# Kernel optimization log

Hardware: AMD Instinct MI355X
Metric: run time of the kernel (lower is better)

Reference implementation:

```python
import jax, jax.numpy as jnp
import numpy as np

T = 4096      # tokens
H = 1024      # hidden_size
I = 4096      # intermediate_size
E = 8         # num_experts


def setup_inputs() -> dict:
    key = jax.random.key(0)
    ks = jax.random.split(key, 6)
    s_h = 1.0 / np.sqrt(H)
    s_i = 1.0 / np.sqrt(I)
    return {
        "x":  jax.random.normal(ks[0], (T, H), dtype=jnp.float32),
        "Wg": jax.random.uniform(ks[1], (E, H), jnp.float32, -s_h, s_h),   # gate: Linear(H, E), no bias
        "W1": jax.random.uniform(ks[2], (E, H, I), jnp.float32, -s_h, s_h),
        "b1": jax.random.uniform(ks[3], (E, I), jnp.float32, -s_h, s_h),
        "W2": jax.random.uniform(ks[4], (E, I, H), jnp.float32, -s_i, s_i),
        "b2": jax.random.uniform(ks[5], (E, H), jnp.float32, -s_i, s_i),
    }


def reference(x, Wg, W1, b1, W2, b2):
    # Gate: softmax over experts. gate_scores: [T, E]
    gate_scores = jax.nn.softmax(x @ Wg.T, axis=-1)
    # All experts run densely on all tokens (batched GEMMs).
    h = jax.nn.gelu(jnp.einsum('th,ehi->eti', x, W1) + b1[:, None, :],
                    approximate=False)                      # [E, T, I]
    y = jnp.einsum('eti,eih->eth', h, W2) + b2[:, None, :]  # [E, T, H]
    # Gate-weighted sum over experts (fuses the stack + mul + sum).
    return jnp.einsum('te,eth->th', gate_scores, y)         # [T, H]
```

## Files before the change

### kernel.cpp

```cpp
#include <hip/hip_runtime.h>
#include <math.h>

#define T_TOK 4096
#define H_DIM 1024
#define I_DIM 4096
#define E_NUM 8
#define KEI   32768


typedef short s16x8 __attribute__((ext_vector_type(8)));
typedef float f32x4 __attribute__((ext_vector_type(4)));

__device__ __forceinline__ unsigned short f2b(float f) {
  union { float f; unsigned u; } v; v.f = f;
  unsigned r = v.u + 0x7fffu + ((v.u >> 16) & 1u);
  return (unsigned short)(r >> 16);
}

__device__ __forceinline__ void gld_lds16(short* lds, const short* g) {
  __builtin_amdgcn_global_load_lds(
      (const __attribute__((address_space(1))) void*)g,
      (__attribute__((address_space(3))) void*)lds, 16, 0, 0);
}

__device__ __forceinline__ float gelu_f(float v) {
  float a = fabsf(v);
  float z = a * 0.70710678118f;
  float t = __builtin_amdgcn_rcpf(fmaf(0.47047f, z, 1.0f));
  float p = fmaf(fmaf(0.7478556f, t, -0.0958798f), t, 0.3480242f) * t;
  float e = __expf(-z * z);
  float erf_abs = fmaf(-p, e, 1.0f);
  return fmaf(0.5f * a, erf_abs, 0.5f * v);
}

__global__ __launch_bounds__(256) void gate_kernel(
    const float* __restrict__ x, const float* __restrict__ Wg,
    float* __restrict__ gate)
{
  int t = blockIdx.x * 4 + (threadIdx.x >> 6);
  int lane = threadIdx.x & 63;
  const float* xr = x + (size_t)t * H_DIM;
  float acc[E_NUM];
#pragma unroll
  for (int e = 0; e < E_NUM; ++e) acc[e] = 0.f;
  for (int j = 0; j < H_DIM / 64; ++j) {
    float xv = xr[lane + j * 64];
#pragma unroll
    for (int e = 0; e < E_NUM; ++e)
      acc[e] += xv * Wg[e * H_DIM + lane + j * 64];
  }
#pragma unroll
  for (int e = 0; e < E_NUM; ++e)
    for (int s = 32; s > 0; s >>= 1)
      acc[e] += __shfl_xor(acc[e], s, 64);
  if (lane == 0) {
    float mx = acc[0];
#pragma unroll
    for (int e = 1; e < E_NUM; ++e) mx = fmaxf(mx, acc[e]);
    float sum = 0.f, ex[E_NUM];
#pragma unroll
    for (int e = 0; e < E_NUM; ++e) { ex[e] = expf(acc[e] - mx); sum += ex[e]; }
    float inv = 1.f / sum;
#pragma unroll
    for (int e = 0; e < E_NUM; ++e) gate[t * E_NUM + e] = ex[e] * inv;
  }
}

__global__ __launch_bounds__(256) void convert_x_kernel(
    const float* __restrict__ x, short* __restrict__ xb)
{
  int rb = blockIdx.x;
  int t  = threadIdx.x & 63;
  int kq = threadIdx.x >> 6;
#pragma unroll
  for (int j = 0; j < 8; ++j) {
    int kc = blockIdx.y * 32 + kq + j * 4;
    const float* src = x + ((size_t)rb * 64 + t) * H_DIM + kc * 8;
    float4 a = *(const float4*)src;
    float4 b = *(const float4*)(src + 4);
    s16x8 v;
    v[0] = f2b(a.x); v[1] = f2b(a.y); v[2] = f2b(a.z); v[3] = f2b(a.w);
    v[4] = f2b(b.x); v[5] = f2b(b.y); v[6] = f2b(b.z); v[7] = f2b(b.w);
    *(s16x8*)(xb + ((size_t)rb * 128 + kc) * 512 + t * 8) = v;
  }
}

__global__ __launch_bounds__(256) void trans_w1_kernel(
    const float* __restrict__ W1, short* __restrict__ W1t)
{
  __shared__ short tile[64][65];
  int e = blockIdx.z;
  int i0 = blockIdx.x * 64, h0 = blockIdx.y * 64;
  int tid = threadIdx.x, c = tid & 63, r0 = tid >> 6;
  const float* src = W1 + ((size_t)e * H_DIM + h0) * I_DIM + i0;
#pragma unroll
  for (int j = 0; j < 16; ++j) {
    int r = j * 4 + r0;
    tile[r][c] = f2b(src[(size_t)r * I_DIM + c]);
  }
  __syncthreads();
  int i = tid & 63, kq = tid >> 6;
#pragma unroll
  for (int w = 0; w < 2; ++w) {
    int kcl = kq + w * 4;
    s16x8 v;
#pragma unroll
    for (int j = 0; j < 8; ++j) v[j] = tile[kcl * 8 + j][i];
    size_t chunk = (size_t)e * 8192 + (size_t)blockIdx.x * 128 + (h0 >> 3) + kcl;
    *(s16x8*)(W1t + chunk * 512 + i * 8) = v;
  }
}

__global__ __launch_bounds__(256) void trans_w2_kernel(
    const float* __restrict__ W2, short* __restrict__ W2t)
{
  __shared__ short tile[64][65];
  int e = blockIdx.z;
  int i0 = blockIdx.x * 64, h0 = blockIdx.y * 64;
  int tid = threadIdx.x, c = tid & 63, r0 = tid >> 6;
  const float* src = W2 + ((size_t)e * I_DIM + i0) * H_DIM + h0;
#pragma unroll
  for (int j = 0; j < 16; ++j) {
    int r = j * 4 + r0;
    tile[r][c] = f2b(src[(size_t)r * H_DIM + c]);
  }
  __syncthreads();
  int h = tid & 63, kq = tid >> 6;
#pragma unroll
  for (int w = 0; w < 2; ++w) {
    int kcl = kq + w * 4;
    s16x8 v;
#pragma unroll
    for (int j = 0; j < 8; ++j) v[j] = tile[kcl * 8 + j][h];
    size_t chunk = (size_t)blockIdx.y * 4096 + e * 512 + (i0 >> 3) + kcl;
    *(s16x8*)(W2t + chunk * 512 + h * 8) = v;
  }
}

__global__ __launch_bounds__(256) void out_init_kernel(
    const float* __restrict__ gate, const float* __restrict__ b2,
    float* __restrict__ out)
{
  int idx = blockIdx.x * 256 + threadIdx.x;
  int t = idx >> 10, h = idx & 1023;
  float v = 0.f;
#pragma unroll
  for (int e = 0; e < E_NUM; ++e)
    v += gate[t * E_NUM + e] * b2[e * H_DIM + h];
  out[idx] = v;
}

__global__ __launch_bounds__(256, 4) void gemm1_kernel(
    const short* __restrict__ xb, const short* __restrict__ W1t,
    const float* __restrict__ b1, const float* __restrict__ gate,
    short* __restrict__ hg)
{
  __shared__ __align__(16) short As[2 * 4096];
  __shared__ __align__(16) short Bs[2 * 4096];
  int bm = blockIdx.x, bn = blockIdx.y, e = blockIdx.z;

  const int tid = threadIdx.x, wave = tid >> 6, lane = tid & 63;
  const int wm = wave >> 1, wn = wave & 1;
  const int g = lane >> 4, r16 = lane & 15;

  f32x4 acc[4][4];
#pragma unroll
  for (int i = 0; i < 4; ++i)
#pragma unroll
    for (int j = 0; j < 4; ++j) acc[i][j] = (f32x4){0.f, 0.f, 0.f, 0.f};

  const int rbl = wave & 1, kq = wave >> 1;
  short* AsD0 = As + (kq * 128 + rbl * 64) * 8;
  short* AsD1 = As + ((kq + 2) * 128 + rbl * 64) * 8;
  short* BsD0 = Bs + (kq * 128 + rbl * 64) * 8;
  short* BsD1 = Bs + ((kq + 2) * 128 + rbl * 64) * 8;
  const short* Asrc = xb + (((size_t)(bm * 2 + rbl) * 128) + kq) * 512 + lane * 8;
  const short* Bsrc = W1t + (size_t)e * (8192 * 512)
                    + (((size_t)(bn * 2 + rbl) * 128) + kq) * 512 + lane * 8;

  gld_lds16(AsD0, Asrc);
  gld_lds16(AsD1, Asrc + 1024);
  gld_lds16(BsD0, Bsrc);
  gld_lds16(BsD1, Bsrc + 1024);

  for (int k0 = 0; k0 < H_DIM; k0 += 32) {
    int cur = (k0 >> 5) & 1;
    __syncthreads();
    if (k0 + 32 < H_DIM) {
      int nb = cur ^ 1;
      size_t soff = ((size_t)(k0 >> 3) + 4) * 512;
      gld_lds16(AsD0 + nb * 4096, Asrc + soff);
      gld_lds16(AsD1 + nb * 4096, Asrc + soff + 1024);
      gld_lds16(BsD0 + nb * 4096, Bsrc + soff);
      gld_lds16(BsD1 + nb * 4096, Bsrc + soff + 1024);
    }
    const short* Ab = As + cur * 4096;
    const short* Bb = Bs + cur * 4096;
    s16x8 af[4], bfr[4];
#pragma unroll
    for (int mi = 0; mi < 4; ++mi)
      af[mi] = *(const s16x8*)(Bb + ((g << 7) + (wm << 6) + (mi << 4) + r16) * 8);
#pragma unroll
    for (int ni = 0; ni < 4; ++ni)
      bfr[ni] = *(const s16x8*)(Ab + ((g << 7) + (wn << 6) + (ni << 4) + r16) * 8);
#pragma unroll
    for (int mi = 0; mi < 4; ++mi)
#pragma unroll
      for (int ni = 0; ni < 4; ++ni)
        acc[mi][ni] = __builtin_amdgcn_mfma_f32_16x16x32_bf16(
            af[mi], bfr[ni], acc[mi][ni], 0, 0, 0);
  }

  int n_base0 = bn * 128 + wm * 64;
  int t_base  = bm * 128 + wn * 64;
  float gt[4];
#pragma unroll
  for (int ni = 0; ni < 4; ++ni)
    gt[ni] = gate[(t_base + ni * 16 + r16) * E_NUM + e];
#pragma unroll
  for (int mi = 0; mi < 4; ++mi) {
    int nb = n_base0 + mi * 16 + g * 4;
    float4 b1v = *(const float4*)(b1 + e * I_DIM + nb);
    int k = e * I_DIM + nb;
    size_t koff = (size_t)(k >> 3) * 512 + (k & 7);
#pragma unroll
    for (int ni = 0; ni < 4; ++ni) {
      int t = t_base + ni * 16 + r16;
      float v0 = gelu_f(acc[mi][ni][0] + b1v.x) * gt[ni];
      float v1 = gelu_f(acc[mi][ni][1] + b1v.y) * gt[ni];
      float v2 = gelu_f(acc[mi][ni][2] + b1v.z) * gt[ni];
      float v3 = gelu_f(acc[mi][ni][3] + b1v.w) * gt[ni];
      int2 pk;
      pk.x = (int)((unsigned)f2b(v0) | ((unsigned)f2b(v1) << 16));
      pk.y = (int)((unsigned)f2b(v2) | ((unsigned)f2b(v3) << 16));
      *(int2*)(hg + (size_t)(t >> 6) * (4096 * 512) + koff + (size_t)(t & 63) * 8) = pk;
    }
  }
}

__global__ __launch_bounds__(256) void gemm2_kernel(
    const short* __restrict__ hg, const short* __restrict__ W2t,
    float* __restrict__ out)
{
  __shared__ __align__(16) short As[2 * 4096];
  __shared__ __align__(16) short Bs[2 * 8192];

  int bn = blockIdx.x;
  int bm = blockIdx.y;
  int ks = blockIdx.z;

  const int tid = threadIdx.x, wave = tid >> 6, lane = tid & 63;
  const int wm = wave >> 1, wn = wave & 1;
  const int g = lane >> 4, r16 = lane & 15;

  f32x4 acc[4][8];
#pragma unroll
  for (int i = 0; i < 4; ++i)
#pragma unroll
    for (int j = 0; j < 8; ++j) acc[i][j] = (f32x4){0.f, 0.f, 0.f, 0.f};

  const int kq = wave;
  short* AsD[2];
  const short* Asrc[2];
#pragma unroll
  for (int r = 0; r < 2; ++r) {
    AsD[r]  = As + (kq * 128 + r * 64) * 8;
    Asrc[r] = hg + (((size_t)(bm * 2 + r) * 4096) + kq) * 512 + lane * 8;
  }
  short* BsD[4];
  const short* Bsrc[4];
#pragma unroll
  for (int r = 0; r < 4; ++r) {
    BsD[r]  = Bs + (kq * 256 + r * 64) * 8;
    Bsrc[r] = W2t + (((size_t)(bn * 4 + r) * 4096) + kq) * 512 + lane * 8;
  }

  const int kBeg = ks * (KEI / 8), kEnd = kBeg + (KEI / 8);

  {
    size_t soff = (size_t)(kBeg >> 3) * 512;
#pragma unroll
    for (int r = 0; r < 2; ++r) gld_lds16(AsD[r], Asrc[r] + soff);
#pragma unroll
    for (int r = 0; r < 4; ++r) gld_lds16(BsD[r], Bsrc[r] + soff);
  }

  for (int k0 = kBeg; k0 < kEnd; k0 += 32) {
    int cur = ((k0 - kBeg) >> 5) & 1;
    __syncthreads();
    if (k0 + 32 < kEnd) {
      int nb = cur ^ 1;
      size_t soff = ((size_t)(k0 >> 3) + 4) * 512;
#pragma unroll
      for (int r = 0; r < 2; ++r) gld_lds16(AsD[r] + nb * 4096, Asrc[r] + soff);
#pragma unroll
      for (int r = 0; r < 4; ++r) gld_lds16(BsD[r] + nb * 8192, Bsrc[r] + soff);
    }
    const short* Ab = As + cur * 4096;
    const short* Bb = Bs + cur * 8192;
    s16x8 af[4], bfr[8];
#pragma unroll
    for (int mi = 0; mi < 4; ++mi)
      af[mi] = *(const s16x8*)(Ab + ((g << 7) + (wm << 6) + (mi << 4) + r16) * 8);
#pragma unroll
    for (int ni = 0; ni < 8; ++ni)
      bfr[ni] = *(const s16x8*)(Bb + ((g << 8) + (wn << 7) + (ni << 4) + r16) * 8);
#pragma unroll
    for (int mi = 0; mi < 4; ++mi)
#pragma unroll
      for (int ni = 0; ni < 8; ++ni)
        acc[mi][ni] = __builtin_amdgcn_mfma_f32_16x16x32_bf16(
            af[mi], bfr[ni], acc[mi][ni], 0, 0, 0);
  }

  int row0 = bm * 128 + wm * 64;
  int col0 = bn * 256 + wn * 128;
#pragma unroll
  for (int mi = 0; mi < 4; ++mi) {
#pragma unroll
    for (int r = 0; r < 4; ++r) {
      int t = row0 + mi * 16 + g * 4 + r;
#pragma unroll
      for (int ni = 0; ni < 8; ++ni) {
        int h = col0 + ni * 16 + r16;
        atomicAdd(&out[(size_t)t * H_DIM + h], acc[mi][ni][r]);
      }
    }
  }
}

extern "C" void kernel_launch(void* const* d_in, const int* in_sizes, int n_in,
                              void* d_out, int out_size, void* d_ws, size_t ws_size,
                              hipStream_t stream) {
  const float* x  = (const float*)d_in[0];
  const float* Wg = (const float*)d_in[1];
  const float* W1 = (const float*)d_in[2];
  const float* b1 = (const float*)d_in[3];
  const float* W2 = (const float*)d_in[4];
  const float* b2 = (const float*)d_in[5];
  float* out = (float*)d_out;

  char* ws = (char*)d_ws;
  float* gate = (float*)ws;
  short* xb   = (short*)(ws + 131072);
  short* W1t  = (short*)(ws + 131072 + 8388608);
  short* W2t  = (short*)(ws + 131072 + 8388608 + 67108864);
  short* hg   = (short*)(ws + 131072 + 8388608 + 2 * 67108864);

  gate_kernel<<<T_TOK / 4, 256, 0, stream>>>(x, Wg, gate);
  convert_x_kernel<<<dim3(T_TOK / 64, 4), 256, 0, stream>>>(x, xb);
  trans_w1_kernel<<<dim3(I_DIM / 64, H_DIM / 64, E_NUM), 256, 0, stream>>>(W1, W1t);
  trans_w2_kernel<<<dim3(I_DIM / 64, H_DIM / 64, E_NUM), 256, 0, stream>>>(W2, W2t);
  out_init_kernel<<<(T_TOK * H_DIM) / 256, 256, 0, stream>>>(gate, b2, out);
  gemm1_kernel<<<dim3(T_TOK / 128, I_DIM / 128, E_NUM), 256, 0, stream>>>(
      xb, W1t, b1, gate, hg);
  gemm2_kernel<<<dim3(4, 32, 8), 256, 0, stream>>>(hg, W2t, out);
}
```

Baseline: 1.014 ms.

## Rewrite expert GEMMs with 256x256 swizzled LDS tiles and split-K reduce

Both GEMMs share a new 512-thread core using 256x256 output tiles, 128KB of dynamic LDS with an XOR swizzle, and a hand-scheduled double-buffered pipeline. It uses global_load_lds prefetch, explicit waitcnt and barriers, and s_setprio around the MFMA bursts. The weight transposes, x conversion and hg epilogue write new tile-contiguous layouts that match this core. The gemm2 float atomicAdd epilogue becomes plain stores of four split-K partial buffers plus a reduce kernel that folds in the gated b2 bias. The aim is higher MFMA utilisation and less LDS and atomic traffic, at the cost of lower occupancy and a partial buffer that overlays the xb and W1t workspace.

```diff
diff --git a/kernel.cpp b/kernel.cpp
--- a/kernel.cpp
+++ b/kernel.cpp
@@ -5,7 +5,6 @@
 #define H_DIM 1024
 #define I_DIM 4096
 #define E_NUM 8
-#define KEI   32768
 
 
 typedef short s16x8 __attribute__((ext_vector_type(8)));
@@ -69,29 +68,28 @@
 __global__ __launch_bounds__(256) void convert_x_kernel(
     const float* __restrict__ x, short* __restrict__ xb)
 {
-  int rb = blockIdx.x;
-  int t  = threadIdx.x & 63;
-  int kq = threadIdx.x >> 6;
-#pragma unroll
-  for (int j = 0; j < 8; ++j) {
-    int kc = blockIdx.y * 32 + kq + j * 4;
-    const float* src = x + ((size_t)rb * 64 + t) * H_DIM + kc * 8;
-    float4 a = *(const float4*)src;
-    float4 b = *(const float4*)(src + 4);
-    s16x8 v;
-    v[0] = f2b(a.x); v[1] = f2b(a.y); v[2] = f2b(a.z); v[3] = f2b(a.w);
-    v[4] = f2b(b.x); v[5] = f2b(b.y); v[6] = f2b(b.z); v[7] = f2b(b.w);
-    *(s16x8*)(xb + ((size_t)rb * 128 + kc) * 512 + t * 8) = v;
-  }
+  int idx = blockIdx.x * 256 + threadIdx.x;
+  int t = idx >> 7;
+  int h0 = (idx & 127) << 3;
+  const float* src = x + (size_t)t * H_DIM + h0;
+  float4 a = *(const float4*)src;
+  float4 b = *(const float4*)(src + 4);
+  s16x8 v;
+  v[0] = f2b(a.x); v[1] = f2b(a.y); v[2] = f2b(a.z); v[3] = f2b(a.w);
+  v[4] = f2b(b.x); v[5] = f2b(b.y); v[6] = f2b(b.z); v[7] = f2b(b.w);
+  int rb = t >> 8, kt = h0 >> 6, half = (t >> 7) & 1;
+  size_t off = ((size_t)((rb * 16 + kt) * 2 + half)) * 8192
+             + (size_t)(t & 127) * 64 + (h0 & 63);
+  *(s16x8*)(xb + off) = v;
 }
 
 __global__ __launch_bounds__(256) void trans_w1_kernel(
     const float* __restrict__ W1, short* __restrict__ W1t)
 {
   __shared__ short tile[64][65];
-  int e = blockIdx.z;
-  int i0 = blockIdx.x * 64, h0 = blockIdx.y * 64;
-  int tid = threadIdx.x, c = tid & 63, r0 = tid >> 6;
+  const int e = blockIdx.z;
+  const int i0 = blockIdx.x * 64, h0 = blockIdx.y * 64;
+  const int tid = threadIdx.x, c = tid & 63, r0 = tid >> 6;
   const float* src = W1 + ((size_t)e * H_DIM + h0) * I_DIM + i0;
 #pragma unroll
   for (int j = 0; j < 16; ++j) {
@@ -99,15 +97,17 @@
     tile[r][c] = f2b(src[(size_t)r * I_DIM + c]);
   }
   __syncthreads();
-  int i = tid & 63, kq = tid >> 6;
+  const int i = tid & 63, kq = tid >> 6;
+  const size_t base = ((size_t)((e * 16 + (i0 >> 8)) * 16 + (h0 >> 6)) * 2
+                       + ((i0 >> 7) & 1)) * 8192
+                    + (size_t)((i0 & 64) + i) * 64;
 #pragma unroll
   for (int w = 0; w < 2; ++w) {
     int kcl = kq + w * 4;
     s16x8 v;
 #pragma unroll
     for (int j = 0; j < 8; ++j) v[j] = tile[kcl * 8 + j][i];
-    size_t chunk = (size_t)e * 8192 + (size_t)blockIdx.x * 128 + (h0 >> 3) + kcl;
-    *(s16x8*)(W1t + chunk * 512 + i * 8) = v;
+    *(s16x8*)(W1t + base + kcl * 8) = v;
   }
 }
 
@@ -115,9 +115,9 @@
     const float* __restrict__ W2, short* __restrict__ W2t)
 {
   __shared__ short tile[64][65];
-  int e = blockIdx.z;
-  int i0 = blockIdx.x * 64, h0 = blockIdx.y * 64;
-  int tid = threadIdx.x, c = tid & 63, r0 = tid >> 6;
+  const int e = blockIdx.z;
+  const int i0 = blockIdx.x * 64, h0 = blockIdx.y * 64;
+  const int tid = threadIdx.x, c = tid & 63, r0 = tid >> 6;
   const float* src = W2 + ((size_t)e * I_DIM + i0) * H_DIM + h0;
 #pragma unroll
   for (int j = 0; j < 16; ++j) {
@@ -125,208 +125,245 @@
     tile[r][c] = f2b(src[(size_t)r * H_DIM + c]);
   }
   __syncthreads();
-  int h = tid & 63, kq = tid >> 6;
+  const int h = tid & 63, kq = tid >> 6;
+  const size_t base = ((size_t)((h0 >> 8) * 512 + e * 64 + (i0 >> 6)) * 2
+                       + ((h0 >> 7) & 1)) * 8192
+                    + (size_t)((h0 & 64) + h) * 64;
 #pragma unroll
   for (int w = 0; w < 2; ++w) {
     int kcl = kq + w * 4;
     s16x8 v;
 #pragma unroll
     for (int j = 0; j < 8; ++j) v[j] = tile[kcl * 8 + j][h];
-    size_t chunk = (size_t)blockIdx.y * 4096 + e * 512 + (i0 >> 3) + kcl;
-    *(s16x8*)(W2t + chunk * 512 + h * 8) = v;
-  }
-}
-
-__global__ __launch_bounds__(256) void out_init_kernel(
-    const float* __restrict__ gate, const float* __restrict__ b2,
-    float* __restrict__ out)
-{
-  int idx = blockIdx.x * 256 + threadIdx.x;
-  int t = idx >> 10, h = idx & 1023;
-  float v = 0.f;
-#pragma unroll
-  for (int e = 0; e < E_NUM; ++e)
-    v += gate[t * E_NUM + e] * b2[e * H_DIM + h];
-  out[idx] = v;
-}
-
-__global__ __launch_bounds__(256, 4) void gemm1_kernel(
+    *(s16x8*)(W2t + base + kcl * 8) = v;
+  }
+}
+
+
+#define BARR()  __builtin_amdgcn_s_barrier()
+#define FENCE() asm volatile("" ::: "memory")
+#define LGKM0() do { asm volatile("s_waitcnt lgkmcnt(0)" ::: "memory"); \
+                     __builtin_amdgcn_sched_barrier(0); } while (0)
+#define VMC(N)  asm volatile("s_waitcnt vmcnt(" #N ")" ::: "memory")
+#define PRIO1() __builtin_amdgcn_s_setprio(1)
+#define PRIO0() __builtin_amdgcn_s_setprio(0)
+#define SCHEDB() __builtin_amdgcn_sched_barrier(0)
+
+__device__ __forceinline__ void gemm_core(
+    const short* __restrict__ Ag, const short* __restrict__ Bg,
+    int nk, short* lds, f32x4 acc[8][4])
+{
+  const int tid  = threadIdx.x;
+  const int wave = tid >> 6, lane = tid & 63;
+  const int wm = wave >> 2, wn = wave & 3;
+  const int g = lane >> 4, r16 = lane & 15;
+
+  const int L0 = tid * 16;
+  const int L1 = 8192 + tid * 16;
+  const int s0 = (L0 ^ (((L0 >> 7) & 7) << 4)) >> 1;
+  const int s1 = (L1 ^ (((L1 >> 7) & 7) << 4)) >> 1;
+
+  short* stA = lds + wave * 512;
+  short* stB = lds + 32768 + wave * 512;
+
+  const int xr_ = (r16 & 7) << 4;
+  const int rd0 = r16 * 64 + ((((0 << 6) | (g << 4)) ^ xr_) >> 1);
+  const int rd1 = r16 * 64 + ((((1 << 6) | (g << 4)) ^ xr_) >> 1);
+
+  const short* Ah = lds + wm * 8192;
+  const short* Bh = lds + 32768 + (wn >> 1) * 8192 + (wn & 1) * 4096;
+
+  s16x8 af[16], bf0, bf1;
+
+#define STAGE_A(KT, HH, BUF) do { \
+    const short* _s = Ag + (size_t)(KT) * 16384 + (HH) * 8192; \
+    short* _d = stA + ((BUF) * 2 + (HH)) * 8192; \
+    gld_lds16(_d, _s + s0); \
+    gld_lds16(_d + 4096, _s + s1); } while (0)
+#define STAGE_B(KT, HH, BUF) do { \
+    const short* _s = Bg + (size_t)(KT) * 16384 + (HH) * 8192; \
+    short* _d = stB + ((BUF) * 2 + (HH)) * 8192; \
+    gld_lds16(_d, _s + s0); \
+    gld_lds16(_d + 4096, _s + s1); } while (0)
+#define LDA(BUF) \
+    _Pragma("unroll") \
+    for (int mi = 0; mi < 8; ++mi) { \
+      af[mi * 2]     = *(const s16x8*)(Ah + (BUF) * 16384 + mi * 1024 + rd0); \
+      af[mi * 2 + 1] = *(const s16x8*)(Ah + (BUF) * 16384 + mi * 1024 + rd1); }
+#define LDB(BUF, NL) do { \
+    bf0 = *(const s16x8*)(Bh + (BUF) * 16384 + (NL) * 1024 + rd0); \
+    bf1 = *(const s16x8*)(Bh + (BUF) * 16384 + (NL) * 1024 + rd1); } while (0)
+#define MFMA_COL(NL) \
+    _Pragma("unroll") \
+    for (int mi = 0; mi < 8; ++mi) { \
+      acc[mi][NL] = __builtin_amdgcn_mfma_f32_16x16x32_bf16(af[mi * 2], bf0, acc[mi][NL], 0, 0, 0); \
+      acc[mi][NL] = __builtin_amdgcn_mfma_f32_16x16x32_bf16(af[mi * 2 + 1], bf1, acc[mi][NL], 0, 0, 0); }
+
+  STAGE_A(0, 0, 0); STAGE_A(0, 1, 0); STAGE_B(0, 0, 0); STAGE_B(0, 1, 0);
+  STAGE_A(1, 0, 1); STAGE_A(1, 1, 1);
+  VMC(4);
+  BARR(); FENCE();
+
+  const int iters = nk >> 1;
+  for (int it = 0; it < iters; ++it) {
+    const int u = it * 2, v = u + 1;
+    const bool nlast = (it + 1 < iters);
+
+    LDA(0); LDB(0, 0);
+    STAGE_B(v, 0, 1);
+    BARR(); LGKM0();
+    PRIO1(); MFMA_COL(0); PRIO0();
+    SCHEDB(); BARR(); FENCE();
+
+    LDB(0, 1);
+    STAGE_B(v, 1, 1);
+    BARR(); LGKM0();
+    PRIO1(); MFMA_COL(1); PRIO0();
+    SCHEDB(); BARR(); FENCE();
+
+    LDB(0, 2);
+    if (nlast) STAGE_A(u + 2, 0, 0);
+    BARR(); LGKM0();
+    PRIO1(); MFMA_COL(2); PRIO0();
+    SCHEDB(); BARR(); FENCE();
+
+    LDB(0, 3);
+    if (nlast) STAGE_A(u + 2, 1, 0);
+    BARR(); LGKM0();
+    PRIO1(); MFMA_COL(3); PRIO0();
+    if (nlast) { VMC(4); } else { VMC(0); }
+    SCHEDB(); BARR(); FENCE();
+
+    LDA(1); LDB(1, 0);
+    if (nlast) STAGE_B(u + 2, 0, 0);
+    BARR(); LGKM0();
+    PRIO1(); MFMA_COL(0); PRIO0();
+    SCHEDB(); BARR(); FENCE();
+
+    LDB(1, 1);
+    if (nlast) STAGE_B(u + 2, 1, 0);
+    BARR(); LGKM0();
+    PRIO1(); MFMA_COL(1); PRIO0();
+    SCHEDB(); BARR(); FENCE();
+
+    LDB(1, 2);
+    if (nlast) STAGE_A(v + 2, 0, 1);
+    BARR(); LGKM0();
+    PRIO1(); MFMA_COL(2); PRIO0();
+    SCHEDB(); BARR(); FENCE();
+
+    LDB(1, 3);
+    if (nlast) STAGE_A(v + 2, 1, 1);
+    BARR(); LGKM0();
+    PRIO1(); MFMA_COL(3); PRIO0();
+    if (nlast) VMC(4);
+    SCHEDB(); BARR(); FENCE();
+  }
+#undef STAGE_A
+#undef STAGE_B
+#undef LDA
+#undef LDB
+#undef MFMA_COL
+}
+
+__global__ __launch_bounds__(512) void gemm1_kernel(
     const short* __restrict__ xb, const short* __restrict__ W1t,
     const float* __restrict__ b1, const float* __restrict__ gate,
     short* __restrict__ hg)
 {
-  __shared__ __align__(16) short As[2 * 4096];
-  __shared__ __align__(16) short Bs[2 * 4096];
-  int bm = blockIdx.x, bn = blockIdx.y, e = blockIdx.z;
+  extern __shared__ short lds[];
+  const int bi = blockIdx.x, bt = blockIdx.y, e = blockIdx.z;
+  f32x4 acc[8][4];
+#pragma unroll
+  for (int i = 0; i < 8; ++i)
+#pragma unroll
+    for (int j = 0; j < 4; ++j) acc[i][j] = (f32x4){0.f, 0.f, 0.f, 0.f};
+
+  const short* Ag = W1t + (size_t)(e * 16 + bi) * 16 * 16384;
+  const short* Bg = xb + (size_t)bt * 16 * 16384;
+  gemm_core(Ag, Bg, 16, lds, acc);
 
   const int tid = threadIdx.x, wave = tid >> 6, lane = tid & 63;
-  const int wm = wave >> 1, wn = wave & 1;
-  const int g = lane >> 4, r16 = lane & 15;
-
-  f32x4 acc[4][4];
-#pragma unroll
-  for (int i = 0; i < 4; ++i)
-#pragma unroll
-    for (int j = 0; j < 4; ++j) acc[i][j] = (f32x4){0.f, 0.f, 0.f, 0.f};
-
-  const int rbl = wave & 1, kq = wave >> 1;
-  short* AsD0 = As + (kq * 128 + rbl * 64) * 8;
-  short* AsD1 = As + ((kq + 2) * 128 + rbl * 64) * 8;
-  short* BsD0 = Bs + (kq * 128 + rbl * 64) * 8;
-  short* BsD1 = Bs + ((kq + 2) * 128 + rbl * 64) * 8;
-  const short* Asrc = xb + (((size_t)(bm * 2 + rbl) * 128) + kq) * 512 + lane * 8;
-  const short* Bsrc = W1t + (size_t)e * (8192 * 512)
-                    + (((size_t)(bn * 2 + rbl) * 128) + kq) * 512 + lane * 8;
-
-  gld_lds16(AsD0, Asrc);
-  gld_lds16(AsD1, Asrc + 1024);
-  gld_lds16(BsD0, Bsrc);
-  gld_lds16(BsD1, Bsrc + 1024);
-
-  for (int k0 = 0; k0 < H_DIM; k0 += 32) {
-    int cur = (k0 >> 5) & 1;
-    __syncthreads();
-    if (k0 + 32 < H_DIM) {
-      int nb = cur ^ 1;
-      size_t soff = ((size_t)(k0 >> 3) + 4) * 512;
-      gld_lds16(AsD0 + nb * 4096, Asrc + soff);
-      gld_lds16(AsD1 + nb * 4096, Asrc + soff + 1024);
-      gld_lds16(BsD0 + nb * 4096, Bsrc + soff);
-      gld_lds16(BsD1 + nb * 4096, Bsrc + soff + 1024);
-    }
-    const short* Ab = As + cur * 4096;
-    const short* Bb = Bs + cur * 4096;
-    s16x8 af[4], bfr[4];
-#pragma unroll
-    for (int mi = 0; mi < 4; ++mi)
-      af[mi] = *(const s16x8*)(Bb + ((g << 7) + (wm << 6) + (mi << 4) + r16) * 8);
-#pragma unroll
-    for (int ni = 0; ni < 4; ++ni)
-      bfr[ni] = *(const s16x8*)(Ab + ((g << 7) + (wn << 6) + (ni << 4) + r16) * 8);
-#pragma unroll
-    for (int mi = 0; mi < 4; ++mi)
-#pragma unroll
-      for (int ni = 0; ni < 4; ++ni)
-        acc[mi][ni] = __builtin_amdgcn_mfma_f32_16x16x32_bf16(
-            af[mi], bfr[ni], acc[mi][ni], 0, 0, 0);
-  }
-
-  int n_base0 = bn * 128 + wm * 64;
-  int t_base  = bm * 128 + wn * 64;
-  float gt[4];
-#pragma unroll
-  for (int ni = 0; ni < 4; ++ni)
-    gt[ni] = gate[(t_base + ni * 16 + r16) * E_NUM + e];
-#pragma unroll
-  for (int mi = 0; mi < 4; ++mi) {
-    int nb = n_base0 + mi * 16 + g * 4;
-    float4 b1v = *(const float4*)(b1 + e * I_DIM + nb);
-    int k = e * I_DIM + nb;
-    size_t koff = (size_t)(k >> 3) * 512 + (k & 7);
-#pragma unroll
-    for (int ni = 0; ni < 4; ++ni) {
-      int t = t_base + ni * 16 + r16;
-      float v0 = gelu_f(acc[mi][ni][0] + b1v.x) * gt[ni];
-      float v1 = gelu_f(acc[mi][ni][1] + b1v.y) * gt[ni];
-      float v2 = gelu_f(acc[mi][ni][2] + b1v.z) * gt[ni];
-      float v3 = gelu_f(acc[mi][ni][3] + b1v.w) * gt[ni];
+  const int wm = wave >> 2, wn = wave & 3, g = lane >> 4, r16 = lane & 15;
+#pragma unroll
+  for (int mg = 0; mg < 8; ++mg) {
+    const int i4 = bi * 256 + wm * 128 + mg * 16 + g * 4;
+    const float4 b1v = *(const float4*)(b1 + e * I_DIM + i4);
+    const int kt = (e * I_DIM + i4) >> 6;
+    const int c = i4 & 63;
+    short* dst = hg + ((size_t)(bt * 512 + kt) * 2 + (wn >> 1)) * 8192 + c;
+#pragma unroll
+    for (int ng = 0; ng < 4; ++ng) {
+      const int tl = wn * 64 + ng * 16 + r16;
+      const float gt = gate[(bt * 256 + tl) * E_NUM + e];
+      const float v0 = gelu_f(acc[mg][ng][0] + b1v.x) * gt;
+      const float v1 = gelu_f(acc[mg][ng][1] + b1v.y) * gt;
+      const float v2 = gelu_f(acc[mg][ng][2] + b1v.z) * gt;
+      const float v3 = gelu_f(acc[mg][ng][3] + b1v.w) * gt;
       int2 pk;
       pk.x = (int)((unsigned)f2b(v0) | ((unsigned)f2b(v1) << 16));
       pk.y = (int)((unsigned)f2b(v2) | ((unsigned)f2b(v3) << 16));
-      *(int2*)(hg + (size_t)(t >> 6) * (4096 * 512) + koff + (size_t)(t & 63) * 8) = pk;
+      *(int2*)(dst + (size_t)(tl & 127) * 64) = pk;
     }
   }
 }
 
-__global__ __launch_bounds__(256) void gemm2_kernel(
-    const short* __restrict__ hg, const short* __restrict__ W2t,
-    float* __restrict__ out)
-{
-  __shared__ __align__(16) short As[2 * 4096];
-  __shared__ __align__(16) short Bs[2 * 8192];
-
-  int bn = blockIdx.x;
-  int bm = blockIdx.y;
-  int ks = blockIdx.z;
+__global__ __launch_bounds__(512) void gemm2_kernel(
+    const short* __restrict__ W2t, const short* __restrict__ hg,
+    float* __restrict__ part)
+{
+  extern __shared__ short lds[];
+  const int bh = blockIdx.x, bt = blockIdx.y, ks = blockIdx.z;
+  f32x4 acc[8][4];
+#pragma unroll
+  for (int i = 0; i < 8; ++i)
+#pragma unroll
+    for (int j = 0; j < 4; ++j) acc[i][j] = (f32x4){0.f, 0.f, 0.f, 0.f};
+
+  const short* Ag = W2t + (size_t)(bh * 512 + ks * 128) * 16384;
+  const short* Bg = hg  + (size_t)(bt * 512 + ks * 128) * 16384;
+  gemm_core(Ag, Bg, 128, lds, acc);
 
   const int tid = threadIdx.x, wave = tid >> 6, lane = tid & 63;
-  const int wm = wave >> 1, wn = wave & 1;
-  const int g = lane >> 4, r16 = lane & 15;
-
-  f32x4 acc[4][8];
-#pragma unroll
-  for (int i = 0; i < 4; ++i)
-#pragma unroll
-    for (int j = 0; j < 8; ++j) acc[i][j] = (f32x4){0.f, 0.f, 0.f, 0.f};
-
-  const int kq = wave;
-  short* AsD[2];
-  const short* Asrc[2];
-#pragma unroll
-  for (int r = 0; r < 2; ++r) {
-    AsD[r]  = As + (kq * 128 + r * 64) * 8;
-    Asrc[r] = hg + (((size_t)(bm * 2 + r) * 4096) + kq) * 512 + lane * 8;
-  }
-  short* BsD[4];
-  const short* Bsrc[4];
-#pragma unroll
-  for (int r = 0; r < 4; ++r) {
-    BsD[r]  = Bs + (kq * 256 + r * 64) * 8;
-    Bsrc[r] = W2t + (((size_t)(bn * 4 + r) * 4096) + kq) * 512 + lane * 8;
-  }
-
-  const int kBeg = ks * (KEI / 8), kEnd = kBeg + (KEI / 8);
-
-  {
-    size_t soff = (size_t)(kBeg >> 3) * 512;
-#pragma unroll
-    for (int r = 0; r < 2; ++r) gld_lds16(AsD[r], Asrc[r] + soff);
-#pragma unroll
-    for (int r = 0; r < 4; ++r) gld_lds16(BsD[r], Bsrc[r] + soff);
-  }
-
-  for (int k0 = kBeg; k0 < kEnd; k0 += 32) {
-    int cur = ((k0 - kBeg) >> 5) & 1;
-    __syncthreads();
-    if (k0 + 32 < kEnd) {
-      int nb = cur ^ 1;
-      size_t soff = ((size_t)(k0 >> 3) + 4) * 512;
-#pragma unroll
-      for (int r = 0; r < 2; ++r) gld_lds16(AsD[r] + nb * 4096, Asrc[r] + soff);
-#pragma unroll
-      for (int r = 0; r < 4; ++r) gld_lds16(BsD[r] + nb * 8192, Bsrc[r] + soff);
+  const int wm = wave >> 2, wn = wave & 3, g = lane >> 4, r16 = lane & 15;
+  float* dst = part + (size_t)ks * ((size_t)T_TOK * H_DIM);
+#pragma unroll
+  for (int mg = 0; mg < 8; ++mg) {
+    const int h4 = bh * 256 + wm * 128 + mg * 16 + g * 4;
+#pragma unroll
+    for (int ng = 0; ng < 4; ++ng) {
+      const int t = bt * 256 + wn * 64 + ng * 16 + r16;
+      *(f32x4*)(dst + (size_t)t * H_DIM + h4) = acc[mg][ng];
     }
-    const short* Ab = As + cur * 4096;
-    const short* Bb = Bs + cur * 8192;
-    s16x8 af[4], bfr[8];
-#pragma unroll
-    for (int mi = 0; mi < 4; ++mi)
-      af[mi] = *(const s16x8*)(Ab + ((g << 7) + (wm << 6) + (mi << 4) + r16) * 8);
-#pragma unroll
-    for (int ni = 0; ni < 8; ++ni)
-      bfr[ni] = *(const s16x8*)(Bb + ((g << 8) + (wn << 7) + (ni << 4) + r16) * 8);
-#pragma unroll
-    for (int mi = 0; mi < 4; ++mi)
-#pragma unroll
-      for (int ni = 0; ni < 8; ++ni)
-        acc[mi][ni] = __builtin_amdgcn_mfma_f32_16x16x32_bf16(
-            af[mi], bfr[ni], acc[mi][ni], 0, 0, 0);
-  }
-
-  int row0 = bm * 128 + wm * 64;
-  int col0 = bn * 256 + wn * 128;
-#pragma unroll
-  for (int mi = 0; mi < 4; ++mi) {
-#pragma unroll
-    for (int r = 0; r < 4; ++r) {
-      int t = row0 + mi * 16 + g * 4 + r;
-#pragma unroll
-      for (int ni = 0; ni < 8; ++ni) {
-        int h = col0 + ni * 16 + r16;
-        atomicAdd(&out[(size_t)t * H_DIM + h], acc[mi][ni][r]);
-      }
-    }
-  }
+  }
+}
+
+__global__ __launch_bounds__(256) void reduce_kernel(
+    const float* __restrict__ part, const float* __restrict__ gate,
+    const float* __restrict__ b2, float* __restrict__ out)
+{
+  const int idx = blockIdx.x * 256 + threadIdx.x;
+  const int t = idx >> 8;
+  const int h4 = (idx & 255) << 2;
+  const size_t off = (size_t)t * H_DIM + h4;
+  const size_t SL = (size_t)T_TOK * H_DIM;
+  float4 a0 = *(const float4*)(part + off);
+  float4 a1 = *(const float4*)(part + SL + off);
+  float4 a2 = *(const float4*)(part + 2 * SL + off);
+  float4 a3 = *(const float4*)(part + 3 * SL + off);
+  float sx = a0.x + a1.x + a2.x + a3.x;
+  float sy = a0.y + a1.y + a2.y + a3.y;
+  float sz = a0.z + a1.z + a2.z + a3.z;
+  float sw = a0.w + a1.w + a2.w + a3.w;
+#pragma unroll
+  for (int e = 0; e < E_NUM; ++e) {
+    const float gv = gate[t * E_NUM + e];
+    const float4 bv = *(const float4*)(b2 + e * H_DIM + h4);
+    sx = fmaf(gv, bv.x, sx); sy = fmaf(gv, bv.y, sy);
+    sz = fmaf(gv, bv.z, sz); sw = fmaf(gv, bv.w, sw);
+  }
+  float4 r; r.x = sx; r.y = sy; r.z = sz; r.w = sw;
+  *(float4*)(out + off) = r;
 }
 
 extern "C" void kernel_launch(void* const* d_in, const int* in_sizes, int n_in,
@@ -346,13 +383,22 @@
   short* W1t  = (short*)(ws + 131072 + 8388608);
   short* W2t  = (short*)(ws + 131072 + 8388608 + 67108864);
   short* hg   = (short*)(ws + 131072 + 8388608 + 2 * 67108864);
+  float* part = (float*)(ws + 131072);
+
+  static bool attr_done = false;
+  if (!attr_done) {
+    hipFuncSetAttribute((const void*)gemm1_kernel,
+                        hipFuncAttributeMaxDynamicSharedMemorySize, 131072);
+    hipFuncSetAttribute((const void*)gemm2_kernel,
+                        hipFuncAttributeMaxDynamicSharedMemorySize, 131072);
+    attr_done = true;
+  }
 
   gate_kernel<<<T_TOK / 4, 256, 0, stream>>>(x, Wg, gate);
-  convert_x_kernel<<<dim3(T_TOK / 64, 4), 256, 0, stream>>>(x, xb);
+  convert_x_kernel<<<2048, 256, 0, stream>>>(x, xb);
   trans_w1_kernel<<<dim3(I_DIM / 64, H_DIM / 64, E_NUM), 256, 0, stream>>>(W1, W1t);
   trans_w2_kernel<<<dim3(I_DIM / 64, H_DIM / 64, E_NUM), 256, 0, stream>>>(W2, W2t);
-  out_init_kernel<<<(T_TOK * H_DIM) / 256, 256, 0, stream>>>(gate, b2, out);
-  gemm1_kernel<<<dim3(T_TOK / 128, I_DIM / 128, E_NUM), 256, 0, stream>>>(
-      xb, W1t, b1, gate, hg);
-  gemm2_kernel<<<dim3(4, 32, 8), 256, 0, stream>>>(hg, W2t, out);
-}
+  gemm1_kernel<<<dim3(16, 16, 8), 512, 131072, stream>>>(xb, W1t, b1, gate, hg);
+  gemm2_kernel<<<dim3(4, 16, 4), 512, 131072, stream>>>(W2t, hg, part);
+  reduce_kernel<<<4096, 256, 0, stream>>>(part, gate, b2, out);
+}
```

Result: faster. 893.8 us (-11.8%).
